# Kernel tuning notes

Hardware: AMD Instinct MI355X
Metric: run time of the kernel (lower is better)

The kernel has to match this reference:

```python
import jax, jax.numpy as jnp
import numpy as np

T, B, E, H = 1024, 8, 1024, 16
DH = E // H
MASKED_BIAS = -10000.0


def setup_inputs() -> dict:
    key = jax.random.key(0)
    k1, k2, k3 = jax.random.split(key, 3)
    query = jax.random.normal(k1, (T, B, E), dtype=jnp.float32)
    # xavier-uniform-ish scale for the fused QKV and output projections
    qkv_w = jax.random.normal(k2, (3 * E, E), dtype=jnp.float32) * (1.0 / np.sqrt(2.0 * E))
    out_w = jax.random.normal(k3, (E, E), dtype=jnp.float32) * (1.0 / np.sqrt(E))
    return {
        "query": query,
        "qkv_w": qkv_w,
        "qkv_b": jnp.zeros((3 * E,), jnp.float32),
        "out_w": out_w,
        "out_b": jnp.zeros((E,), jnp.float32),
    }


def reference(query, qkv_w, qkv_b, out_w, out_b):
    # query: [T, B, E] (Time x Batch x Channel, fairseq convention)
    tgt_len, bsz, embed_dim = query.shape
    scaling = DH ** (-0.5)

    # Fused QKV projection (QuantLinear fake-quant treated as identity numerics)
    qkv = jnp.einsum("tbe,fe->tbf", query, qkv_w) + qkv_b  # [T, B, 3E]
    q, k, v = jnp.split(qkv, 3, axis=-1)
    q = q * scaling

    def to_heads(x):  # [T, B, E] -> [B*H, T, DH]
        return x.reshape(tgt_len, bsz * H, DH).transpose(1, 0, 2)

    q, k, v = to_heads(q), to_heads(k), to_heads(v)

    # attn_weights: [B*H, T, S]
    attn_weights = jnp.einsum("ntd,nsd->nts", q, k)

    # causal mask from the tril `bias` buffer with masked_bias fill
    causal = jnp.tril(jnp.ones((tgt_len, tgt_len), dtype=bool))
    attn_weights = jnp.where(causal[None, :, :], attn_weights,
                             jnp.asarray(MASKED_BIAS, attn_weights.dtype))

    attn_probs = jax.nn.softmax(attn_weights, axis=-1)
    # dropout p=0.0 in eval: no-op

    attn = jnp.einsum("nts,nsd->ntd", attn_probs, v)  # [B*H, T, DH]
    attn = attn.transpose(1, 0, 2).reshape(tgt_len, bsz, embed_dim)  # [T, B, E]

    out = jnp.einsum("tbe,fe->tbf", attn, out_w) + out_b
    return out
```

## Files before the change

kernel.cpp:

```cpp
#include <hip/hip_runtime.h>

typedef __attribute__((ext_vector_type(4))) float f32x4;
typedef __attribute__((ext_vector_type(16))) float f32x16;
typedef __attribute__((ext_vector_type(8))) short bf16x8;
typedef __attribute__((ext_vector_type(4))) unsigned short u16x4;
typedef __attribute__((ext_vector_type(4))) unsigned int u32x4;

#define T_DIM 1024
#define B_DIM 8
#define E_DIM 1024
#define H_DIM 16
#define DH 64

__device__ __forceinline__ unsigned short f2bf(float f) {
  unsigned int u = __builtin_bit_cast(unsigned int, f);
  u += 0x7fffu + ((u >> 16) & 1u);
  return (unsigned short)(u >> 16);
}

__device__ __forceinline__ unsigned int cvtpk_bf16(float lo, float hi) {
  unsigned int r;
  asm("v_cvt_pk_bf16_f32 %0, %1, %2" : "=v"(r) : "v"(lo), "v"(hi));
  return r;
}

__device__ __forceinline__ float exp2_hw(float x) {
  float r;
  asm("v_exp_f32 %0, %1" : "=v"(r) : "v"(x));
  return r;
}

__device__ __forceinline__ f32x4 mfma16(bf16x8 a, bf16x8 b, f32x4 c) {
  return __builtin_amdgcn_mfma_f32_16x16x32_bf16(a, b, c, 0, 0, 0);
}
__device__ __forceinline__ f32x16 mfma32(bf16x8 a, bf16x8 b, f32x16 c) {
  return __builtin_amdgcn_mfma_f32_32x32x16_bf16(a, b, c, 0, 0, 0);
}

__global__ __launch_bounds__(256) void cast_f32_to_bf16(
    const float* __restrict__ src, unsigned short* __restrict__ dst, int n4) {
  int i = blockIdx.x * 256 + threadIdx.x;
  if (i >= n4) return;
  f32x4 v = *(const f32x4*)(src + (size_t)i * 4);
  u16x4 o;
  o[0] = f2bf(v[0]); o[1] = f2bf(v[1]); o[2] = f2bf(v[2]); o[3] = f2bf(v[3]);
  *(u16x4*)(dst + (size_t)i * 4) = o;
}

__device__ __forceinline__ void gemm_mainloop(
    const unsigned short* __restrict__ A, const unsigned short* __restrict__ B,
    int K, int m0, int n0, unsigned short* lA, unsigned short* lB, f32x4 acc[4][4]) {
  const int tid = threadIdx.x;
  const int wave = tid >> 6, lane = tid & 63;
  const int lr = lane & 15, lg = lane >> 4;
  const int wr = wave >> 1, wc = wave & 1;
  const int o0 = wave * 1024 + lane * 16;
  for (int k0 = 0; k0 < K; k0 += 32) {
    if (k0) __syncthreads();
#pragma unroll
    for (int c = 0; c < 2; ++c) {
      const int o = c * 4096 + o0;
      const int row = o >> 6;
      const int ce = (o & 63) >> 1;
      __builtin_amdgcn_global_load_lds(
          (const __attribute__((address_space(1))) void*)(A + (size_t)(m0 + row) * K + k0 + ce),
          (__attribute__((address_space(3))) void*)(lA + c * 2048 + wave * 512), 16, 0, 0);
      __builtin_amdgcn_global_load_lds(
          (const __attribute__((address_space(1))) void*)(B + (size_t)(n0 + row) * K + k0 + ce),
          (__attribute__((address_space(3))) void*)(lB + c * 2048 + wave * 512), 16, 0, 0);
    }
    __syncthreads();
    bf16x8 af[4], bfr[4];
#pragma unroll
    for (int i = 0; i < 4; ++i) {
      af[i]  = *(const bf16x8*)(lA + (wr * 64 + i * 16 + lr) * 32 + lg * 8);
      bfr[i] = *(const bf16x8*)(lB + (wc * 64 + i * 16 + lr) * 32 + lg * 8);
    }
#pragma unroll
    for (int mi = 0; mi < 4; ++mi)
#pragma unroll
      for (int ni = 0; ni < 4; ++ni)
        acc[mi][ni] = mfma16(af[mi], bfr[ni], acc[mi][ni]);
  }
}

__global__ __launch_bounds__(256) void gemm_qkv(
    const unsigned short* __restrict__ A, const unsigned short* __restrict__ W,
    const float* __restrict__ bias,
    unsigned short* __restrict__ Qh, unsigned short* __restrict__ Kh,
    unsigned short* __restrict__ Vh) {
  __shared__ unsigned short lA[4096], lB[4096];
  f32x4 acc[4][4];
  const f32x4 z4 = {0.f, 0.f, 0.f, 0.f};
#pragma unroll
  for (int i = 0; i < 4; ++i)
#pragma unroll
    for (int j = 0; j < 4; ++j) acc[i][j] = z4;
  const int m0 = blockIdx.x * 128, n0 = blockIdx.y * 128;
  gemm_mainloop(A, W, 1024, m0, n0, lA, lB, acc);

  const int lane = threadIdx.x & 63, wave = threadIdx.x >> 6;
  const int lr = lane & 15, lg = lane >> 4;
  const int wr = wave >> 1, wc = wave & 1;
#pragma unroll
  for (int mi = 0; mi < 4; ++mi)
#pragma unroll
    for (int ni = 0; ni < 4; ++ni)
#pragma unroll
      for (int j = 0; j < 4; ++j) {
        int m = m0 + wr * 64 + mi * 16 + lg * 4 + j;
        int f = n0 + wc * 64 + ni * 16 + lr;
        float v = acc[mi][ni][j] + bias[f];
        int t = m >> 3, b = m & 7;
        int e = f & 1023, h = e >> 6, d = e & 63;
        int which = f >> 10;
        size_t idx = ((size_t)(b * 16 + h) * T_DIM + t) * DH + d;
        if (which == 0)      Qh[idx] = f2bf(v * 0.18033688011111772f);
        else if (which == 1) Kh[idx] = f2bf(v);
        else                 Vh[idx] = f2bf(v);
      }
}

__global__ __launch_bounds__(256) void transpose_v(
    const unsigned short* __restrict__ Vh, unsigned short* __restrict__ Vt) {
  __shared__ unsigned short tile[64][72];
  const int n = blockIdx.x, t0 = blockIdx.y * 64;
  const int tid = threadIdx.x;
  const int r = tid >> 3, c8 = tid & 7;
#pragma unroll
  for (int it = 0; it < 2; ++it) {
    int row = it * 32 + r;
    bf16x8 v = *(const bf16x8*)(Vh + ((size_t)n * T_DIM + t0 + row) * DH + c8 * 8);
    *(bf16x8*)&tile[row][c8 * 8] = v;
  }
  __syncthreads();
#pragma unroll
  for (int it = 0; it < 2; ++it) {
    int d = it * 32 + r;
    bf16x8 ov;
#pragma unroll
    for (int jj = 0; jj < 8; ++jj) ov[jj] = (short)tile[c8 * 8 + jj][d];
    *(bf16x8*)(Vt + ((size_t)n * DH + d) * T_DIM + t0 + c8 * 8) = ov;
  }
}

__global__ __launch_bounds__(256) void flash_attn6(
    const unsigned short* __restrict__ Qh, const unsigned short* __restrict__ Kh,
    const unsigned short* __restrict__ Vt, unsigned short* __restrict__ attn) {
  __shared__ unsigned short lds[2][2][4096];
  const int tid = threadIdx.x;
  const int wave = tid >> 6, lane = tid & 63;
  const int lq = lane & 31, hi = lane >> 5;
  const int bid = blockIdx.x;
  const int qt = 7 - (bid >> 7);
  const int n = bid & 127;
  const int b = n >> 4, h = n & 15;
  const int q0w = qt * 128 + wave * 32;
  const int q = q0w + lq;
  const int nbb = 2 * qt + 2;
  const int mynb = (q0w + 95) >> 6;

  const unsigned short* kh_n = Kh + (size_t)n * (T_DIM * DH);
  const unsigned short* vt_n = Vt + (size_t)n * (DH * T_DIM);

  const int rlo = lane >> 3;
  const int csw = 8 * ((lane & 7) ^ rlo);

#define STAGE(S0, BUF)                                                          \
  {                                                                             \
    _Pragma("unroll")                                                           \
    for (int m_ = 0; m_ < 2; ++m_) {                                            \
      const int instr_ = wave * 2 + m_;                                         \
      const int r_ = instr_ * 8 + rlo;                                          \
      __builtin_amdgcn_global_load_lds(                                         \
          (const __attribute__((address_space(1))) void*)(kh_n + (size_t)((S0) + r_) * DH + csw), \
          (__attribute__((address_space(3))) void*)(&lds[BUF][0][instr_ * 512]), 16, 0, 0); \
      __builtin_amdgcn_global_load_lds(                                         \
          (const __attribute__((address_space(1))) void*)(vt_n + (size_t)r_ * T_DIM + (S0) + csw), \
          (__attribute__((address_space(3))) void*)(&lds[BUF][1][instr_ * 512]), 16, 0, 0); \
    }                                                                           \
  }

  bf16x8 qf[4];
  const unsigned short* qp = Qh + ((size_t)n * T_DIM + q) * DH + hi * 8;
#pragma unroll
  for (int kk = 0; kk < 4; ++kk) qf[kk] = *(const bf16x8*)(qp + kk * 16);

  f32x16 o0, o1;
#pragma unroll
  for (int r = 0; r < 16; ++r) { o0[r] = 0.f; o1[r] = 0.f; }
  float m_run = -1e30f, l_run = 0.f;

  STAGE(0, 0);
  asm volatile("s_waitcnt vmcnt(0)");
  __builtin_amdgcn_s_barrier();

  const int swz = (lq & 7) << 4;

  for (int i = 0; i < nbb; ++i) {
    const int cur = i & 1;
    if (i + 1 < nbb) {
      STAGE((i + 1) * 64, cur ^ 1);
      asm volatile("s_waitcnt vmcnt(4)");
    } else {
      asm volatile("s_waitcnt vmcnt(0)");
    }
    __builtin_amdgcn_s_barrier();
    __builtin_amdgcn_sched_barrier(0);

    if (i < mynb) {
      const int s0 = i * 64;
      const unsigned short* kb = lds[cur][0];
      const unsigned short* vb = lds[cur][1];
      f32x16 sA, sB;
#pragma unroll
      for (int r = 0; r < 16; ++r) { sA[r] = 0.f; sB[r] = 0.f; }
      __builtin_amdgcn_s_setprio(1);
#pragma unroll
      for (int kk = 0; kk < 4; ++kk) {
        const int cb = ((kk * 32 + hi * 16) ^ swz) >> 1;
        bf16x8 ka = *(const bf16x8*)(kb + lq * 64 + cb);
        bf16x8 kbf = *(const bf16x8*)(kb + (32 + lq) * 64 + cb);
        sA = mfma32(ka, qf[kk], sA);
        sB = mfma32(kbf, qf[kk], sB);
      }
      __builtin_amdgcn_s_setprio(0);
      if (i == mynb - 1) {
#pragma unroll
        for (int r = 0; r < 16; ++r) {
          int sp = s0 + (r & 3) + 8 * (r >> 2) + 4 * hi;
          if (sp > q)      sA[r] = -10000.0f;
          if (sp + 32 > q) sB[r] = -10000.0f;
        }
      }
      float t0 = fmaxf(sA[0], sB[0]), t1 = fmaxf(sA[1], sB[1]);
      float t2 = fmaxf(sA[2], sB[2]), t3 = fmaxf(sA[3], sB[3]);
#pragma unroll
      for (int r = 4; r < 16; r += 4) {
        t0 = fmaxf(t0, fmaxf(sA[r], sB[r]));
        t1 = fmaxf(t1, fmaxf(sA[r + 1], sB[r + 1]));
        t2 = fmaxf(t2, fmaxf(sA[r + 2], sB[r + 2]));
        t3 = fmaxf(t3, fmaxf(sA[r + 3], sB[r + 3]));
      }
      float tmax = fmaxf(fmaxf(t0, t1), fmaxf(t2, t3));
      tmax = fmaxf(tmax, __shfl_xor(tmax, 32));
      if (__any(tmax - m_run > 11.5f)) {
        float m_new = fmaxf(m_run, tmax);
        float sc = exp2_hw(m_run - m_new);
        l_run *= sc;
#pragma unroll
        for (int r = 0; r < 16; ++r) { o0[r] *= sc; o1[r] *= sc; }
        m_run = m_new;
      }
      float r0 = 0.f, r1 = 0.f, r2 = 0.f, r3 = 0.f;
#pragma unroll
      for (int r = 0; r < 16; r += 4) {
        sA[r] = exp2_hw(sA[r] - m_run);         r0 += sA[r];
        sA[r + 1] = exp2_hw(sA[r + 1] - m_run); r1 += sA[r + 1];
        sA[r + 2] = exp2_hw(sA[r + 2] - m_run); r2 += sA[r + 2];
        sA[r + 3] = exp2_hw(sA[r + 3] - m_run); r3 += sA[r + 3];
      }
#pragma unroll
      for (int r = 0; r < 16; r += 4) {
        sB[r] = exp2_hw(sB[r] - m_run);         r0 += sB[r];
        sB[r + 1] = exp2_hw(sB[r + 1] - m_run); r1 += sB[r + 1];
        sB[r + 2] = exp2_hw(sB[r + 2] - m_run); r2 += sB[r + 2];
        sB[r + 3] = exp2_hw(sB[r + 3] - m_run); r3 += sB[r + 3];
      }
      float rs = (r0 + r1) + (r2 + r3);
      rs += __shfl_xor(rs, 32);
      l_run += rs;
      unsigned int pk[16];
#pragma unroll
      for (int ii = 0; ii < 8; ++ii) pk[ii]     = cvtpk_bf16(sA[2 * ii], sA[2 * ii + 1]);
#pragma unroll
      for (int ii = 0; ii < 8; ++ii) pk[8 + ii] = cvtpk_bf16(sB[2 * ii], sB[2 * ii + 1]);
      __builtin_amdgcn_s_setprio(1);
#pragma unroll
      for (int ks = 0; ks < 4; ++ks) {
        unsigned int A0 = pk[ks * 4 + 0], A1 = pk[ks * 4 + 1];
        unsigned int B0 = pk[ks * 4 + 2], B1 = pk[ks * 4 + 3];
        unsigned int xA0 = __shfl_xor(A0, 32), xA1 = __shfl_xor(A1, 32);
        unsigned int xB0 = __shfl_xor(B0, 32), xB1 = __shfl_xor(B1, 32);
        u32x4 uu;
        uu[0] = hi ? xB0 : A0;
        uu[1] = hi ? xB1 : A1;
        uu[2] = hi ? B0 : xA0;
        uu[3] = hi ? B1 : xA1;
        bf16x8 pf = __builtin_bit_cast(bf16x8, uu);
        const int cb = ((ks * 32 + hi * 16) ^ swz) >> 1;
        bf16x8 v0 = *(const bf16x8*)(vb + lq * 64 + cb);
        bf16x8 v1 = *(const bf16x8*)(vb + (32 + lq) * 64 + cb);
        o0 = mfma32(v0, pf, o0);
        o1 = mfma32(v1, pf, o1);
      }
      __builtin_amdgcn_s_setprio(0);
    }
    __builtin_amdgcn_s_barrier();
  }
#undef STAGE

  const float inv = 1.0f / l_run;
  unsigned short* op = attn + ((size_t)q * B_DIM + b) * E_DIM + h * DH;
#pragma unroll
  for (int g = 0; g < 4; ++g) {
    u16x4 w0, w1;
#pragma unroll
    for (int jj = 0; jj < 4; ++jj) {
      w0[jj] = f2bf(o0[g * 4 + jj] * inv);
      w1[jj] = f2bf(o1[g * 4 + jj] * inv);
    }
    int d = 8 * g + 4 * hi;
    *(u16x4*)(op + d) = w0;
    *(u16x4*)(op + 32 + d) = w1;
  }
}

__global__ __launch_bounds__(256) void gemm_out(
    const unsigned short* __restrict__ A, const unsigned short* __restrict__ W,
    const float* __restrict__ bias, float* __restrict__ out) {
  __shared__ unsigned short lA[4096], lB[4096];
  f32x4 acc[4][4];
  const f32x4 z4 = {0.f, 0.f, 0.f, 0.f};
#pragma unroll
  for (int i = 0; i < 4; ++i)
#pragma unroll
    for (int j = 0; j < 4; ++j) acc[i][j] = z4;
  const int m0 = blockIdx.x * 128, n0 = blockIdx.y * 128;
  gemm_mainloop(A, W, 1024, m0, n0, lA, lB, acc);

  const int lane = threadIdx.x & 63, wave = threadIdx.x >> 6;
  const int lr = lane & 15, lg = lane >> 4;
  const int wr = wave >> 1, wc = wave & 1;
#pragma unroll
  for (int mi = 0; mi < 4; ++mi)
#pragma unroll
    for (int ni = 0; ni < 4; ++ni)
#pragma unroll
      for (int j = 0; j < 4; ++j) {
        int m = m0 + wr * 64 + mi * 16 + lg * 4 + j;
        int f = n0 + wc * 64 + ni * 16 + lr;
        out[(size_t)m * E_DIM + f] = acc[mi][ni][j] + bias[f];
      }
}

extern "C" void kernel_launch(void* const* d_in, const int* in_sizes, int n_in,
                              void* d_out, int out_size, void* d_ws, size_t ws_size,
                              hipStream_t stream) {
  const float* query = (const float*)d_in[0];
  const float* qkv_w = (const float*)d_in[1];
  const float* qkv_b = (const float*)d_in[2];
  const float* out_w = (const float*)d_in[3];
  const float* out_b = (const float*)d_in[4];
  float* out = (float*)d_out;

  char* ws = (char*)d_ws;
  unsigned short* Abf  = (unsigned short*)(ws);
  unsigned short* Wbf  = (unsigned short*)(ws + (size_t)(16u << 20));
  unsigned short* OWbf = (unsigned short*)(ws + (size_t)(22u << 20));
  unsigned short* Qh   = (unsigned short*)(ws + (size_t)(24u << 20));
  unsigned short* Kh   = (unsigned short*)(ws + (size_t)(40u << 20));
  unsigned short* Vh   = (unsigned short*)(ws + (size_t)(56u << 20));
  unsigned short* Vt   = (unsigned short*)(ws + (size_t)(72u << 20));
  unsigned short* attn = Abf;

  cast_f32_to_bf16<<<8192, 256, 0, stream>>>(query, Abf, 8388608 / 4);
  cast_f32_to_bf16<<<3072, 256, 0, stream>>>(qkv_w, Wbf, 3145728 / 4);
  cast_f32_to_bf16<<<1024, 256, 0, stream>>>(out_w, OWbf, 1048576 / 4);
  gemm_qkv<<<dim3(64, 24), 256, 0, stream>>>(Abf, Wbf, qkv_b, Qh, Kh, Vh);
  transpose_v<<<dim3(128, 16), 256, 0, stream>>>(Vh, Vt);
  flash_attn6<<<1024, 256, 0, stream>>>(Qh, Kh, Vt, attn);
  gemm_out<<<dim3(64, 8), 256, 0, stream>>>(attn, OWbf, out_b, out);
}
```

Measured before the change: 163.5 us.

## Rewrite QKV projection GEMM with 256x256 tiles and staged LDS pipeline

After: 170.0 us. +4.0%, slower.

```diff
diff --git a/kernel.cpp b/kernel.cpp
--- a/kernel.cpp
+++ b/kernel.cpp
@@ -84,33 +84,169 @@
   }
 }
 
-__global__ __launch_bounds__(256) void gemm_qkv(
+__global__ __launch_bounds__(512, 2) void gemm_qkv8(
     const unsigned short* __restrict__ A, const unsigned short* __restrict__ W,
     const float* __restrict__ bias,
     unsigned short* __restrict__ Qh, unsigned short* __restrict__ Kh,
     unsigned short* __restrict__ Vh) {
-  __shared__ unsigned short lA[4096], lB[4096];
-  f32x4 acc[4][4];
+  extern __shared__ unsigned short smem[];
+  unsigned short* lA = smem;
+  unsigned short* lB = smem + 32768;
+
+  const int tid = threadIdx.x;
+  const int wave = tid >> 6, lane = tid & 63;
+  const int lr = lane & 15, lg = lane >> 4;
+  const int x7 = lr & 7;
+  const int wr = wave >> 2, wc = wave & 3;
+  const int w2 = wave * 2;
+  const int rlo = lane >> 3;
+  const int csw = 8 * ((lane & 7) ^ rlo);
+
+  const int bid = blockIdx.x;
+  const int swz = (bid & 7) * 48 + (bid >> 3);
+  const int m0 = (swz & 31) * 256;
+  const int n0 = (swz >> 5) * 256;
+
+  const unsigned short* Asrc = A + (size_t)m0 * 1024;
+  const unsigned short* Bsrc = W + (size_t)n0 * 1024;
+
+#define STAGE1(TT, S)                                                           \
+  {                                                                             \
+    const int buf_ = (TT) & 1;                                                  \
+    const unsigned short* g_;                                                   \
+    unsigned short* l_;                                                         \
+    if ((S) < 2) {                                                              \
+      g_ = Asrc + (size_t)((S) * 128) * 1024 + (TT) * 64;                       \
+      l_ = lA + (buf_ * 2 + (S)) * 8192;                                        \
+    } else {                                                                    \
+      g_ = Bsrc + (size_t)(((S) - 2) * 128) * 1024 + (TT) * 64;                 \
+      l_ = lB + (buf_ * 2 + ((S) - 2)) * 8192;                                  \
+    }                                                                           \
+    _Pragma("unroll")                                                           \
+    for (int c_ = 0; c_ < 2; ++c_) {                                            \
+      const int ins_ = w2 + c_;                                                 \
+      __builtin_amdgcn_global_load_lds(                                         \
+          (const __attribute__((address_space(1))) void*)(g_ + (size_t)(ins_ * 8 + rlo) * 1024 + csw), \
+          (__attribute__((address_space(3))) void*)(l_ + ins_ * 512), 16, 0, 0); \
+    }                                                                           \
+  }
+
+  f32x4 acc[8][4];
   const f32x4 z4 = {0.f, 0.f, 0.f, 0.f};
 #pragma unroll
-  for (int i = 0; i < 4; ++i)
+  for (int i = 0; i < 8; ++i)
 #pragma unroll
     for (int j = 0; j < 4; ++j) acc[i][j] = z4;
-  const int m0 = blockIdx.x * 128, n0 = blockIdx.y * 128;
-  gemm_mainloop(A, W, 1024, m0, n0, lA, lB, acc);
-
-  const int lane = threadIdx.x & 63, wave = threadIdx.x >> 6;
-  const int lr = lane & 15, lg = lane >> 4;
-  const int wr = wave >> 1, wc = wave & 1;
-#pragma unroll
-  for (int mi = 0; mi < 4; ++mi)
-#pragma unroll
-    for (int ni = 0; ni < 4; ++ni)
+
+  STAGE1(0, 0); STAGE1(0, 1); STAGE1(0, 2); STAGE1(0, 3); STAGE1(1, 0);
+  asm volatile("s_waitcnt vmcnt(2)" ::: "memory");
+  __builtin_amdgcn_s_barrier();
+  __builtin_amdgcn_sched_barrier(0);
+
+  for (int t = 0; t < 16; ++t) {
+    const int buf = t & 1;
+    const unsigned short* hA = lA + (buf * 2 + wr) * 8192;
+    const unsigned short* hB = lB + (buf * 2 + (wc >> 1)) * 8192;
+    const int rb = (wc & 1) * 64;
+    bf16x8 af[4][2], bfx[2][2];
+
+#pragma unroll
+    for (int mf = 0; mf < 4; ++mf)
+#pragma unroll
+      for (int ks = 0; ks < 2; ++ks)
+        af[mf][ks] = *(const bf16x8*)(hA + (mf * 16 + lr) * 64 + (((ks * 4 + lg) ^ x7) << 3));
+#pragma unroll
+    for (int nf = 0; nf < 2; ++nf)
+#pragma unroll
+      for (int ks = 0; ks < 2; ++ks)
+        bfx[nf][ks] = *(const bf16x8*)(hB + (rb + nf * 16 + lr) * 64 + (((ks * 4 + lg) ^ x7) << 3));
+    STAGE1(t + 1, 1);
+    __builtin_amdgcn_s_barrier();
+    __builtin_amdgcn_sched_barrier(0);
+    __builtin_amdgcn_s_setprio(1);
+#pragma unroll
+    for (int mf = 0; mf < 4; ++mf)
+#pragma unroll
+      for (int nf = 0; nf < 2; ++nf)
+#pragma unroll
+        for (int ks = 0; ks < 2; ++ks)
+          acc[mf][nf] = mfma16(af[mf][ks], bfx[nf][ks], acc[mf][nf]);
+    __builtin_amdgcn_s_setprio(0);
+    __builtin_amdgcn_s_barrier();
+    __builtin_amdgcn_sched_barrier(0);
+
+#pragma unroll
+    for (int nf = 0; nf < 2; ++nf)
+#pragma unroll
+      for (int ks = 0; ks < 2; ++ks)
+        bfx[nf][ks] = *(const bf16x8*)(hB + (rb + (2 + nf) * 16 + lr) * 64 + (((ks * 4 + lg) ^ x7) << 3));
+    STAGE1(t + 1, 2);
+    __builtin_amdgcn_s_barrier();
+    __builtin_amdgcn_sched_barrier(0);
+    __builtin_amdgcn_s_setprio(1);
+#pragma unroll
+    for (int mf = 0; mf < 4; ++mf)
+#pragma unroll
+      for (int nf = 0; nf < 2; ++nf)
+#pragma unroll
+        for (int ks = 0; ks < 2; ++ks)
+          acc[mf][2 + nf] = mfma16(af[mf][ks], bfx[nf][ks], acc[mf][2 + nf]);
+    __builtin_amdgcn_s_setprio(0);
+    __builtin_amdgcn_s_barrier();
+    __builtin_amdgcn_sched_barrier(0);
+
+#pragma unroll
+    for (int mf = 0; mf < 4; ++mf)
+#pragma unroll
+      for (int ks = 0; ks < 2; ++ks)
+        af[mf][ks] = *(const bf16x8*)(hA + ((4 + mf) * 16 + lr) * 64 + (((ks * 4 + lg) ^ x7) << 3));
+    STAGE1(t + 1, 3);
+    __builtin_amdgcn_s_barrier();
+    __builtin_amdgcn_sched_barrier(0);
+    __builtin_amdgcn_s_setprio(1);
+#pragma unroll
+    for (int mf = 0; mf < 4; ++mf)
+#pragma unroll
+      for (int nf = 0; nf < 2; ++nf)
+#pragma unroll
+        for (int ks = 0; ks < 2; ++ks)
+          acc[4 + mf][2 + nf] = mfma16(af[mf][ks], bfx[nf][ks], acc[4 + mf][2 + nf]);
+    __builtin_amdgcn_s_setprio(0);
+    __builtin_amdgcn_s_barrier();
+    __builtin_amdgcn_sched_barrier(0);
+
+#pragma unroll
+    for (int nf = 0; nf < 2; ++nf)
+#pragma unroll
+      for (int ks = 0; ks < 2; ++ks)
+        bfx[nf][ks] = *(const bf16x8*)(hB + (rb + nf * 16 + lr) * 64 + (((ks * 4 + lg) ^ x7) << 3));
+    STAGE1(t + 2, 0);
+    __builtin_amdgcn_s_barrier();
+    __builtin_amdgcn_sched_barrier(0);
+    __builtin_amdgcn_s_setprio(1);
+#pragma unroll
+    for (int mf = 0; mf < 4; ++mf)
+#pragma unroll
+      for (int nf = 0; nf < 2; ++nf)
+#pragma unroll
+        for (int ks = 0; ks < 2; ++ks)
+          acc[4 + mf][nf] = mfma16(af[mf][ks], bfx[nf][ks], acc[4 + mf][nf]);
+    __builtin_amdgcn_s_setprio(0);
+    asm volatile("s_waitcnt vmcnt(2)" ::: "memory");
+    __builtin_amdgcn_s_barrier();
+    __builtin_amdgcn_sched_barrier(0);
+  }
+#undef STAGE1
+
+#pragma unroll
+  for (int mf = 0; mf < 8; ++mf)
+#pragma unroll
+    for (int nf = 0; nf < 4; ++nf)
 #pragma unroll
       for (int j = 0; j < 4; ++j) {
-        int m = m0 + wr * 64 + mi * 16 + lg * 4 + j;
-        int f = n0 + wc * 64 + ni * 16 + lr;
-        float v = acc[mi][ni][j] + bias[f];
+        int m = m0 + wr * 128 + mf * 16 + lg * 4 + j;
+        int f = n0 + wc * 64 + nf * 16 + lr;
+        float v = acc[mf][nf][j] + bias[f];
         int t = m >> 3, b = m & 7;
         int e = f & 1023, h = e >> 6, d = e & 63;
         int which = f >> 10;
@@ -195,7 +331,7 @@
   asm volatile("s_waitcnt vmcnt(0)");
   __builtin_amdgcn_s_barrier();
 
-  const int swz = (lq & 7) << 4;
+  const int swzr = (lq & 7) << 4;
 
   for (int i = 0; i < nbb; ++i) {
     const int cur = i & 1;
@@ -218,7 +354,7 @@
       __builtin_amdgcn_s_setprio(1);
 #pragma unroll
       for (int kk = 0; kk < 4; ++kk) {
-        const int cb = ((kk * 32 + hi * 16) ^ swz) >> 1;
+        const int cb = ((kk * 32 + hi * 16) ^ swzr) >> 1;
         bf16x8 ka = *(const bf16x8*)(kb + lq * 64 + cb);
         bf16x8 kbf = *(const bf16x8*)(kb + (32 + lq) * 64 + cb);
         sA = mfma32(ka, qf[kk], sA);
@@ -288,7 +424,7 @@
         uu[2] = hi ? B0 : xA0;
         uu[3] = hi ? B1 : xA1;
         bf16x8 pf = __builtin_bit_cast(bf16x8, uu);
-        const int cb = ((ks * 32 + hi * 16) ^ swz) >> 1;
+        const int cb = ((ks * 32 + hi * 16) ^ swzr) >> 1;
         bf16x8 v0 = *(const bf16x8*)(vb + lq * 64 + cb);
         bf16x8 v1 = *(const bf16x8*)(vb + (32 + lq) * 64 + cb);
         o0 = mfma32(v0, pf, o0);
@@ -367,7 +503,7 @@
   cast_f32_to_bf16<<<8192, 256, 0, stream>>>(query, Abf, 8388608 / 4);
   cast_f32_to_bf16<<<3072, 256, 0, stream>>>(qkv_w, Wbf, 3145728 / 4);
   cast_f32_to_bf16<<<1024, 256, 0, stream>>>(out_w, OWbf, 1048576 / 4);
-  gemm_qkv<<<dim3(64, 24), 256, 0, stream>>>(Abf, Wbf, qkv_b, Qh, Kh, Vh);
+  gemm_qkv8<<<384, 512, 131072, stream>>>(Abf, Wbf, qkv_b, Qh, Kh, Vh);
   transpose_v<<<dim3(128, 16), 256, 0, stream>>>(Vh, Vt);
   flash_attn6<<<1024, 256, 0, stream>>>(Qh, Kh, Vt, attn);
   gemm_out<<<dim3(64, 8), 256, 0, stream>>>(attn, OWbf, out_b, out);
```

## Replace both projection GEMMs with 128x256-tile, 3-stage pipelined, swizzled mainloop

Applied to the files above, without the earlier changes.

Result: no change. 161.3 us (-1.4%).

```diff
diff --git a/kernel.cpp b/kernel.cpp
--- a/kernel.cpp
+++ b/kernel.cpp
@@ -47,70 +47,116 @@
   *(u16x4*)(dst + (size_t)i * 4) = o;
 }
 
-__device__ __forceinline__ void gemm_mainloop(
-    const unsigned short* __restrict__ A, const unsigned short* __restrict__ B,
-    int K, int m0, int n0, unsigned short* lA, unsigned short* lB, f32x4 acc[4][4]) {
+__device__ __forceinline__ void mainloop_128x256(
+    const unsigned short* __restrict__ Ab,
+    const unsigned short* __restrict__ Bb,
+    unsigned short* smem, f32x4 acc[4][4]) {
   const int tid = threadIdx.x;
   const int wave = tid >> 6, lane = tid & 63;
   const int lr = lane & 15, lg = lane >> 4;
-  const int wr = wave >> 1, wc = wave & 1;
-  const int o0 = wave * 1024 + lane * 16;
-  for (int k0 = 0; k0 < K; k0 += 32) {
-    if (k0) __syncthreads();
-#pragma unroll
-    for (int c = 0; c < 2; ++c) {
-      const int o = c * 4096 + o0;
-      const int row = o >> 6;
-      const int ce = (o & 63) >> 1;
-      __builtin_amdgcn_global_load_lds(
-          (const __attribute__((address_space(1))) void*)(A + (size_t)(m0 + row) * K + k0 + ce),
-          (__attribute__((address_space(3))) void*)(lA + c * 2048 + wave * 512), 16, 0, 0);
-      __builtin_amdgcn_global_load_lds(
-          (const __attribute__((address_space(1))) void*)(B + (size_t)(n0 + row) * K + k0 + ce),
-          (__attribute__((address_space(3))) void*)(lB + c * 2048 + wave * 512), 16, 0, 0);
-    }
-    __syncthreads();
-    bf16x8 af[4], bfr[4];
-#pragma unroll
-    for (int i = 0; i < 4; ++i) {
-      af[i]  = *(const bf16x8*)(lA + (wr * 64 + i * 16 + lr) * 32 + lg * 8);
-      bfr[i] = *(const bf16x8*)(lB + (wc * 64 + i * 16 + lr) * 32 + lg * 8);
-    }
-#pragma unroll
-    for (int mi = 0; mi < 4; ++mi)
-#pragma unroll
-      for (int ni = 0; ni < 4; ++ni)
-        acc[mi][ni] = mfma16(af[mi], bfr[ni], acc[mi][ni]);
-  }
-}
-
-__global__ __launch_bounds__(256) void gemm_qkv(
+  const int x7 = lr & 7;
+  const int wr = wave >> 2, wc = wave & 3;
+  const int rlo = lane >> 3;
+  const int csw = 8 * ((lane & 7) ^ rlo);
+
+#define STG(KT, BUF)                                                            \
+  {                                                                             \
+    unsigned short* la_ = smem + (BUF) * 24576;                                 \
+    unsigned short* lb_ = la_ + 8192;                                           \
+    _Pragma("unroll")                                                           \
+    for (int c_ = 0; c_ < 2; ++c_) {                                            \
+      const int ins_ = wave * 2 + c_;                                           \
+      __builtin_amdgcn_global_load_lds(                                         \
+          (const __attribute__((address_space(1))) void*)(Ab + (size_t)(ins_ * 8 + rlo) * 1024 + (KT) * 64 + csw), \
+          (__attribute__((address_space(3))) void*)(la_ + ins_ * 512), 16, 0, 0); \
+    }                                                                           \
+    _Pragma("unroll")                                                           \
+    for (int c_ = 0; c_ < 4; ++c_) {                                            \
+      const int ins_ = wave * 4 + c_;                                           \
+      __builtin_amdgcn_global_load_lds(                                         \
+          (const __attribute__((address_space(1))) void*)(Bb + (size_t)(ins_ * 8 + rlo) * 1024 + (KT) * 64 + csw), \
+          (__attribute__((address_space(3))) void*)(lb_ + ins_ * 512), 16, 0, 0); \
+    }                                                                           \
+  }
+
+#define COMPUTE(BUF)                                                            \
+  {                                                                             \
+    const unsigned short* la_ = smem + (BUF) * 24576;                           \
+    const unsigned short* ha_ = la_ + (wr * 64) * 64;                           \
+    const unsigned short* hb_ = la_ + 8192 + (wc * 64) * 64;                    \
+    _Pragma("unroll")                                                           \
+    for (int ks_ = 0; ks_ < 2; ++ks_) {                                         \
+      bf16x8 af_[4], bf_[4];                                                    \
+      const int cu_ = (((ks_ * 4 + lg) ^ x7) << 3);                             \
+      _Pragma("unroll")                                                         \
+      for (int i_ = 0; i_ < 4; ++i_) {                                          \
+        af_[i_] = *(const bf16x8*)(ha_ + (i_ * 16 + lr) * 64 + cu_);            \
+        bf_[i_] = *(const bf16x8*)(hb_ + (i_ * 16 + lr) * 64 + cu_);            \
+      }                                                                         \
+      __builtin_amdgcn_s_setprio(1);                                            \
+      _Pragma("unroll")                                                         \
+      for (int mi_ = 0; mi_ < 4; ++mi_)                                         \
+        _Pragma("unroll")                                                       \
+        for (int ni_ = 0; ni_ < 4; ++ni_)                                       \
+          acc[mi_][ni_] = mfma16(af_[mi_], bf_[ni_], acc[mi_][ni_]);            \
+      __builtin_amdgcn_s_setprio(0);                                            \
+    }                                                                           \
+  }
+
+#define ENDT(WAITSTR)                                                           \
+  asm volatile("s_waitcnt " WAITSTR ::: "memory");                              \
+  __builtin_amdgcn_s_barrier();                                                 \
+  __builtin_amdgcn_sched_barrier(0);
+
+  STG(0, 0) STG(1, 1)
+  ENDT("vmcnt(6)")
+
+  for (int tt = 0; tt < 12; tt += 3) {
+    STG(tt + 2, 2) COMPUTE(0) ENDT("vmcnt(6)")
+    STG(tt + 3, 0) COMPUTE(1) ENDT("vmcnt(6)")
+    STG(tt + 4, 1) COMPUTE(2) ENDT("vmcnt(6)")
+  }
+  STG(14, 2) COMPUTE(0) ENDT("vmcnt(6)")
+  STG(15, 0) COMPUTE(1) ENDT("vmcnt(6)")
+  COMPUTE(2) ENDT("vmcnt(0)")
+  COMPUTE(0)
+#undef STG
+#undef COMPUTE
+#undef ENDT
+}
+
+__global__ __launch_bounds__(512) void gemm_qkv9(
     const unsigned short* __restrict__ A, const unsigned short* __restrict__ W,
     const float* __restrict__ bias,
     unsigned short* __restrict__ Qh, unsigned short* __restrict__ Kh,
     unsigned short* __restrict__ Vh) {
-  __shared__ unsigned short lA[4096], lB[4096];
+  extern __shared__ unsigned short smem[];
+  const int bid = blockIdx.x;
+  const int swz = (bid & 7) * 96 + (bid >> 3);
+  const int m0 = (swz & 63) * 128;
+  const int n0 = (swz >> 6) * 256;
+
   f32x4 acc[4][4];
   const f32x4 z4 = {0.f, 0.f, 0.f, 0.f};
 #pragma unroll
   for (int i = 0; i < 4; ++i)
 #pragma unroll
     for (int j = 0; j < 4; ++j) acc[i][j] = z4;
-  const int m0 = blockIdx.x * 128, n0 = blockIdx.y * 128;
-  gemm_mainloop(A, W, 1024, m0, n0, lA, lB, acc);
+
+  mainloop_128x256(A + (size_t)m0 * 1024, W + (size_t)n0 * 1024, smem, acc);
 
   const int lane = threadIdx.x & 63, wave = threadIdx.x >> 6;
   const int lr = lane & 15, lg = lane >> 4;
-  const int wr = wave >> 1, wc = wave & 1;
-#pragma unroll
-  for (int mi = 0; mi < 4; ++mi)
-#pragma unroll
-    for (int ni = 0; ni < 4; ++ni)
+  const int wr = wave >> 2, wc = wave & 3;
+#pragma unroll
+  for (int mf = 0; mf < 4; ++mf)
+#pragma unroll
+    for (int nf = 0; nf < 4; ++nf)
 #pragma unroll
       for (int j = 0; j < 4; ++j) {
-        int m = m0 + wr * 64 + mi * 16 + lg * 4 + j;
-        int f = n0 + wc * 64 + ni * 16 + lr;
-        float v = acc[mi][ni][j] + bias[f];
+        int m = m0 + wr * 64 + mf * 16 + lg * 4 + j;
+        int f = n0 + wc * 64 + nf * 16 + lr;
+        float v = acc[mf][nf][j] + bias[f];
         int t = m >> 3, b = m & 7;
         int e = f & 1023, h = e >> 6, d = e & 63;
         int which = f >> 10;
@@ -118,6 +164,39 @@
         if (which == 0)      Qh[idx] = f2bf(v * 0.18033688011111772f);
         else if (which == 1) Kh[idx] = f2bf(v);
         else                 Vh[idx] = f2bf(v);
+      }
+}
+
+__global__ __launch_bounds__(512) void gemm_out9(
+    const unsigned short* __restrict__ A, const unsigned short* __restrict__ W,
+    const float* __restrict__ bias, float* __restrict__ out) {
+  extern __shared__ unsigned short smem[];
+  const int bid = blockIdx.x;
+  const int swz = (bid & 7) * 32 + (bid >> 3);
+  const int m0 = (swz & 63) * 128;
+  const int n0 = (swz >> 6) * 256;
+
+  f32x4 acc[4][4];
+  const f32x4 z4 = {0.f, 0.f, 0.f, 0.f};
+#pragma unroll
+  for (int i = 0; i < 4; ++i)
+#pragma unroll
+    for (int j = 0; j < 4; ++j) acc[i][j] = z4;
+
+  mainloop_128x256(A + (size_t)m0 * 1024, W + (size_t)n0 * 1024, smem, acc);
+
+  const int lane = threadIdx.x & 63, wave = threadIdx.x >> 6;
+  const int lr = lane & 15, lg = lane >> 4;
+  const int wr = wave >> 2, wc = wave & 3;
+#pragma unroll
+  for (int mf = 0; mf < 4; ++mf)
+#pragma unroll
+    for (int nf = 0; nf < 4; ++nf)
+#pragma unroll
+      for (int j = 0; j < 4; ++j) {
+        int m = m0 + wr * 64 + mf * 16 + lg * 4 + j;
+        int f = n0 + wc * 64 + nf * 16 + lr;
+        out[(size_t)m * E_DIM + f] = acc[mf][nf][j] + bias[f];
       }
 }
 
@@ -195,7 +274,7 @@
   asm volatile("s_waitcnt vmcnt(0)");
   __builtin_amdgcn_s_barrier();
 
-  const int swz = (lq & 7) << 4;
+  const int swzr = (lq & 7) << 4;
 
   for (int i = 0; i < nbb; ++i) {
     const int cur = i & 1;
@@ -218,7 +297,7 @@
       __builtin_amdgcn_s_setprio(1);
 #pragma unroll
       for (int kk = 0; kk < 4; ++kk) {
-        const int cb = ((kk * 32 + hi * 16) ^ swz) >> 1;
+        const int cb = ((kk * 32 + hi * 16) ^ swzr) >> 1;
         bf16x8 ka = *(const bf16x8*)(kb + lq * 64 + cb);
         bf16x8 kbf = *(const bf16x8*)(kb + (32 + lq) * 64 + cb);
         sA = mfma32(ka, qf[kk], sA);
@@ -288,7 +367,7 @@
         uu[2] = hi ? B0 : xA0;
         uu[3] = hi ? B1 : xA1;
         bf16x8 pf = __builtin_bit_cast(bf16x8, uu);
-        const int cb = ((ks * 32 + hi * 16) ^ swz) >> 1;
+        const int cb = ((ks * 32 + hi * 16) ^ swzr) >> 1;
         bf16x8 v0 = *(const bf16x8*)(vb + lq * 64 + cb);
         bf16x8 v1 = *(const bf16x8*)(vb + (32 + lq) * 64 + cb);
         o0 = mfma32(v0, pf, o0);
@@ -314,34 +393,6 @@
     *(u16x4*)(op + d) = w0;
     *(u16x4*)(op + 32 + d) = w1;
   }
-}
-
-__global__ __launch_bounds__(256) void gemm_out(
-    const unsigned short* __restrict__ A, const unsigned short* __restrict__ W,
-    const float* __restrict__ bias, float* __restrict__ out) {
-  __shared__ unsigned short lA[4096], lB[4096];
-  f32x4 acc[4][4];
-  const f32x4 z4 = {0.f, 0.f, 0.f, 0.f};
-#pragma unroll
-  for (int i = 0; i < 4; ++i)
-#pragma unroll
-    for (int j = 0; j < 4; ++j) acc[i][j] = z4;
-  const int m0 = blockIdx.x * 128, n0 = blockIdx.y * 128;
-  gemm_mainloop(A, W, 1024, m0, n0, lA, lB, acc);
-
-  const int lane = threadIdx.x & 63, wave = threadIdx.x >> 6;
-  const int lr = lane & 15, lg = lane >> 4;
-  const int wr = wave >> 1, wc = wave & 1;
-#pragma unroll
-  for (int mi = 0; mi < 4; ++mi)
-#pragma unroll
-    for (int ni = 0; ni < 4; ++ni)
-#pragma unroll
-      for (int j = 0; j < 4; ++j) {
-        int m = m0 + wr * 64 + mi * 16 + lg * 4 + j;
-        int f = n0 + wc * 64 + ni * 16 + lr;
-        out[(size_t)m * E_DIM + f] = acc[mi][ni][j] + bias[f];
-      }
 }
 
 extern "C" void kernel_launch(void* const* d_in, const int* in_sizes, int n_in,
@@ -367,8 +418,8 @@
   cast_f32_to_bf16<<<8192, 256, 0, stream>>>(query, Abf, 8388608 / 4);
   cast_f32_to_bf16<<<3072, 256, 0, stream>>>(qkv_w, Wbf, 3145728 / 4);
   cast_f32_to_bf16<<<1024, 256, 0, stream>>>(out_w, OWbf, 1048576 / 4);
-  gemm_qkv<<<dim3(64, 24), 256, 0, stream>>>(Abf, Wbf, qkv_b, Qh, Kh, Vh);
+  gemm_qkv9<<<768, 512, 147456, stream>>>(Abf, Wbf, qkv_b, Qh, Kh, Vh);
   transpose_v<<<dim3(128, 16), 256, 0, stream>>>(Vh, Vt);
   flash_attn6<<<1024, 256, 0, stream>>>(Qh, Kh, Vt, attn);
-  gemm_out<<<dim3(64, 8), 256, 0, stream>>>(attn, OWbf, out_b, out);
-}
+  gemm_out9<<<256, 512, 147456, stream>>>(attn, OWbf, out_b, out);
+}
```
